# Performance work log

Hardware: AMD Instinct MI355X
Metric: run time of the kernel (lower is better)

## Reference

```python
import jax, jax.numpy as jnp
import numpy as np


def _time_encoding(t, hidden_dim):
    # Sinusoidal continuous-time encoding: t [B,T] -> [B,T,H]
    half = hidden_dim // 2
    freqs = jnp.exp(-jnp.arange(half, dtype=t.dtype) * (np.log(10000.0) / half))
    ang = t[..., None] * freqs  # [B,T,half]
    return jnp.concatenate([jnp.sin(ang), jnp.cos(ang)], axis=-1)


def _gru(x_tbh, w_ih, w_hh, b_ih, b_hh):
    # PyTorch-convention GRU over time-major input [T,B,H]
    B = x_tbh.shape[1]
    H = w_hh.shape[1]
    h0 = jnp.zeros((B, H), x_tbh.dtype)

    def step(h, x):
        gi = x @ w_ih.T + b_ih
        gh = h @ w_hh.T + b_hh
        i_r, i_z, i_n = jnp.split(gi, 3, axis=-1)
        h_r, h_z, h_n = jnp.split(gh, 3, axis=-1)
        r = jax.nn.sigmoid(i_r + h_r)
        z = jax.nn.sigmoid(i_z + h_z)
        n = jnp.tanh(i_n + r * h_n)
        h_new = (1.0 - z) * n + z * h
        return h_new, h_new

    _, ys = jax.lax.scan(step, h0, x_tbh)
    return ys  # [T,B,H]


def setup_inputs():
    key = jax.random.key(0)
    ks = jax.random.split(key, 8)
    B, T, D, H = 32, 256, 64, 128
    x = jax.random.normal(ks[0], (B, T, D), jnp.float32)
    missing_mask = (jax.random.uniform(ks[1], (B, T, D)) < 0.5).astype(jnp.float32)
    visit_time = jnp.cumsum(jax.random.uniform(ks[2], (B, T), jnp.float32) * 2.0, axis=1)
    time_delta = jnp.zeros((B, T), jnp.float32)
    lengths = jax.random.randint(ks[3], (B,), T // 2, T + 1).astype(jnp.int32)
    lengths = lengths.at[0].set(T)  # pad_packed returns max(lengths) steps; pin to T
    sensor_embed = jax.random.normal(ks[4], (D, H), jnp.float32) * 0.02
    k = 1.0 / np.sqrt(H)
    gru_w_ih = jax.random.uniform(ks[5], (3 * H, H), jnp.float32, -k, k)
    gru_w_hh = jax.random.uniform(ks[6], (3 * H, H), jnp.float32, -k, k)
    gru_b_ih = jax.random.uniform(ks[7], (3 * H,), jnp.float32, -k, k)
    gru_b_hh = jnp.zeros((3 * H,), jnp.float32)
    return dict(x=x, missing_mask=missing_mask, visit_time=visit_time,
                time_delta=time_delta, lengths=lengths, sensor_embed=sensor_embed,
                gru_w_ih=gru_w_ih, gru_w_hh=gru_w_hh, gru_b_ih=gru_b_ih, gru_b_hh=gru_b_hh)


def reference(x, missing_mask, visit_time, time_delta, lengths, sensor_embed,
              gru_w_ih, gru_w_hh, gru_b_ih, gru_b_hh):
    B, T, D = x.shape
    H = sensor_embed.shape[1]
    observed = 1.0 - missing_mask                                   # [B,T,D]
    # sensor tokens: per-(t,sensor) embedding scaled by value, zeroed if missing
    sensor_tokens = x[..., None] * sensor_embed[None, None] * observed[..., None]  # [B,T,D,H]
    presence = observed.mean(axis=1)                                # [B,D]
    sim = jax.nn.relu(sensor_embed @ sensor_embed.T)                # [D,D]
    adj = presence[:, :, None] * presence[:, None, :] * sim[None]   # [B,D,D]
    adj = adj + jnp.eye(D, dtype=x.dtype)[None]
    adj = adj / jnp.maximum(adj.sum(axis=-1, keepdims=True), 1e-6)
    graph_tokens = jnp.einsum('bij,btjh->btih', adj, sensor_tokens) # [B,T,D,H]
    visit_repr = graph_tokens.mean(axis=2) + _time_encoding(visit_time, H)  # [B,T,H]
    # dropout is identity in eval mode
    ys = _gru(jnp.swapaxes(visit_repr, 0, 1), gru_w_ih, gru_w_hh, gru_b_ih, gru_b_hh)
    out = jnp.swapaxes(ys, 0, 1)                                    # [B,T,H]
    # pad_packed_sequence semantics: zeros beyond each sequence length
    mask = (jnp.arange(T)[None, :] < lengths[:, None])[..., None]
    return out * mask
```

## Files before the change

kernel.cpp:

```cpp
#include <hip/hip_runtime.h>
#include <hip/hip_bf16.h>

#define B_ 32
#define T_ 256
#define D_ 64
#define H_ 128
#define G_ 384

typedef _Float16 half8 __attribute__((ext_vector_type(8)));
typedef _Float16 half4v __attribute__((ext_vector_type(4)));
typedef float float4v __attribute__((ext_vector_type(4)));

__device__ __forceinline__ float fsigmoid2(float s){
  return __builtin_amdgcn_rcpf(1.0f + __builtin_amdgcn_exp2f(-s));
}
__device__ __forceinline__ float ftanh2(float t){
  return 1.0f - 2.0f*__builtin_amdgcn_rcpf(1.0f + __builtin_amdgcn_exp2f(t));
}
#define LOG2E  1.442695041f
#define LOG2E2 2.885390082f

#define BAR() do{ asm volatile("s_waitcnt lgkmcnt(0)" ::: "memory"); \
                  __builtin_amdgcn_s_barrier(); \
                  asm volatile("" ::: "memory"); } while(0)

__global__ void __launch_bounds__(256) adj_k(const float* mm, const float* E,
                                             float* wcol){
  int b = blockIdx.x;
  int tid = threadIdx.x;
  int d = tid & 63, q = tid >> 6;
  __shared__ float spp[4][64];
  __shared__ float sp[64];
  __shared__ float sE[64*129];
  __shared__ float ssim[64*65];
  __shared__ float srs[64];
  float p = 0.0f;
  for (int t = q*64; t < q*64+64; t++) p += 1.0f - mm[(b*T_ + t)*D_ + d];
  spp[q][d] = p;
  for (int i = tid; i < D_*H_; i += 256){ int r = i >> 7, c = i & 127; sE[r*129+c] = E[i]; }
  __syncthreads();
  if (tid < 64) sp[tid] = (spp[0][tid]+spp[1][tid]+spp[2][tid]+spp[3][tid]) * (1.0f/T_);
  __syncthreads();
  float rowE[128];
  #pragma unroll
  for (int k = 0; k < 128; k++) rowE[k] = sE[d*129+k];
  for (int i = q*16; i < q*16+16; i++){
    float s = 0.0f;
    #pragma unroll
    for (int k = 0; k < 128; k++) s += rowE[k]*sE[i*129+k];
    ssim[d*65+i] = fmaxf(s, 0.0f);
  }
  __syncthreads();
  if (tid < 64){
    float rs = 0.0f;
    for (int j = 0; j < 64; j++) rs += sp[j]*ssim[tid*65+j];
    srs[tid] = fmaxf(sp[tid]*rs + 1.0f, 1e-6f);
  }
  __syncthreads();
  if (tid < 64){
    float s = 0.0f;
    for (int i = 0; i < 64; i++) s += sp[i]*ssim[tid*65+i]/srs[i];
    wcol[b*64 + tid] = sp[tid]*s + 1.0f/srs[tid];
  }
}

#define AVP 72
#define VRP 136
#define SEP 132
__global__ void __launch_bounds__(512,1) gi_k(const float* x, const float* mm,
                                              const float* vt, const float* E,
                                              const float* wih, const float* bih,
                                              const float* bhh, const float* wcol,
                                              _Float16* gi3){
  int bid = blockIdx.x;
  int b = bid >> 3, t0 = (bid & 7)*32;
  int tid = threadIdx.x;
  int w = tid >> 6, l = tid & 63;
  int lq = l >> 4, lm = l & 15;

  __shared__ __align__(16) _Float16 av[32*AVP];
  __shared__ __align__(16) _Float16 vrA[32*VRP];
  __shared__ __align__(16) _Float16 sEl[64*SEP];
  __shared__ float sVt[32];

  {
    int i = tid*4, t = i >> 6, d4 = i & 63;
    long src = (long)(b*T_ + t0 + t)*D_ + d4;
    float4 xv = *(const float4*)&x[src];
    float4 mv = *(const float4*)&mm[src];
    float4 wv = *(const float4*)&wcol[b*D_ + d4];
    half4v h;
    h[0]=(_Float16)(xv.x*(1.0f-mv.x)*wv.x*(1.0f/64));
    h[1]=(_Float16)(xv.y*(1.0f-mv.y)*wv.y*(1.0f/64));
    h[2]=(_Float16)(xv.z*(1.0f-mv.z)*wv.z*(1.0f/64));
    h[3]=(_Float16)(xv.w*(1.0f-mv.w)*wv.w*(1.0f/64));
    *(half4v*)&av[t*AVP + d4] = h;
  }
  {
    int r = tid >> 3, c0 = (tid & 7)*16;
    #pragma unroll
    for (int g = 0; g < 4; g++){
      float4 v = *(const float4*)&E[r*H_ + c0 + g*4];
      half4v h;
      h[0]=(_Float16)v.x; h[1]=(_Float16)v.y; h[2]=(_Float16)v.z; h[3]=(_Float16)v.w;
      *(half4v*)&sEl[r*SEP + c0 + g*4] = h;
    }
  }
  if (tid < 32) sVt[tid] = vt[b*T_ + t0 + tid];
  __syncthreads();

  half8 bE[2];
  #pragma unroll
  for (int kc = 0; kc < 2; kc++){
    half8 f;
    #pragma unroll
    for (int jj = 0; jj < 8; jj++)
      f[jj] = sEl[(kc*32 + lq*8 + jj)*SEP + 16*w + lm];
    bE[kc] = f;
  }

  float4v accA[2] = {{0,0,0,0},{0,0,0,0}};
  #pragma unroll
  for (int kc = 0; kc < 2; kc++){
    #pragma unroll
    for (int mt = 0; mt < 2; mt++){
      half8 a = *(const half8*)&av[(mt*16+lm)*AVP + kc*32 + lq*8];
      accA[mt] = __builtin_amdgcn_mfma_f32_16x16x32_f16(a, bE[kc], accA[mt], 0,0,0);
    }
  }
  {
    int h = 16*w + lm;
    float fr = __expf(-(float)(h & 63) * 0.14391157f);
    #pragma unroll
    for (int mt = 0; mt < 2; mt++){
      #pragma unroll
      for (int r = 0; r < 4; r++){
        int tl = mt*16 + lq*4 + r;
        float ang = sVt[tl] * fr;
        float e = (h < 64) ? __sinf(ang) : __cosf(ang);
        vrA[tl*VRP + h] = (_Float16)(accA[mt][r] + e);
      }
    }
  }
  __syncthreads();

  half8 bW[3][4]; float biW[3];
  #pragma unroll
  for (int q = 0; q < 3; q++){
    int g = 16*(3*w + q) + lm;
    float sc = (g < 2*H_) ? LOG2E : LOG2E2;
    biW[q] = (bih[g] + (g < 2*H_ ? bhh[g] : 0.0f)) * sc;
    #pragma unroll
    for (int kc = 0; kc < 4; kc++){
      const float* src = &wih[(long)g*H_ + kc*32 + lq*8];
      float4 x0 = *(const float4*)src;
      float4 x1 = *(const float4*)(src+4);
      half8 f;
      f[0]=(_Float16)(x0.x*sc); f[1]=(_Float16)(x0.y*sc); f[2]=(_Float16)(x0.z*sc); f[3]=(_Float16)(x0.w*sc);
      f[4]=(_Float16)(x1.x*sc); f[5]=(_Float16)(x1.y*sc); f[6]=(_Float16)(x1.z*sc); f[7]=(_Float16)(x1.w*sc);
      bW[q][kc] = f;
    }
  }
  float4v cB[2][3];
  #pragma unroll
  for (int mt = 0; mt < 2; mt++)
    #pragma unroll
    for (int q = 0; q < 3; q++) cB[mt][q] = (float4v){0,0,0,0};
  #pragma unroll
  for (int kc = 0; kc < 4; kc++){
    #pragma unroll
    for (int mt = 0; mt < 2; mt++){
      half8 a = *(const half8*)&vrA[(mt*16+lm)*VRP + kc*32 + lq*8];
      #pragma unroll
      for (int q = 0; q < 3; q++)
        cB[mt][q] = __builtin_amdgcn_mfma_f32_16x16x32_f16(a, bW[q][kc], cB[mt][q], 0,0,0);
    }
  }
  #pragma unroll
  for (int mt = 0; mt < 2; mt++){
    #pragma unroll
    for (int q = 0; q < 3; q++){
      int g = 16*(3*w + q) + lm;
      int tb = t0 + mt*16 + lq*4;
      half4v hv;
      hv[0]=(_Float16)(cB[mt][q][0] + biW[q]); hv[1]=(_Float16)(cB[mt][q][1] + biW[q]);
      hv[2]=(_Float16)(cB[mt][q][2] + biW[q]); hv[3]=(_Float16)(cB[mt][q][3] + biW[q]);
      *(half4v*)&gi3[((long)(b*G_ + g))*T_ + tb] = hv;
    }
  }
}

__global__ void __launch_bounds__(512,1) gru_k(const _Float16* gi3, const float* whh,
                                               const float* bhh, const int* lengths,
                                               float* out){
  int b = blockIdx.x;
  int tid = threadIdx.x;
  int w = tid >> 6, l = tid & 63;
  int lq = l >> 4;
  int j = 16*w + (l & 15);
  bool gate = (l < 16);
  int len = lengths[b];

  __shared__ __align__(16) _Float16 hb[2][H_];

  half8 bfrag[3][4];
  #pragma unroll
  for (int q = 0; q < 3; q++){
    int row = q*H_ + 16*w + (l & 15);
    float sc = (q == 2) ? LOG2E2 : LOG2E;
    #pragma unroll
    for (int kc = 0; kc < 4; kc++){
      const float* src = &whh[(long)row*H_ + kc*32 + lq*8];
      float4 x0 = *(const float4*)src;
      float4 x1 = *(const float4*)(src+4);
      half8 f;
      f[0]=(_Float16)(x0.x*sc); f[1]=(_Float16)(x0.y*sc); f[2]=(_Float16)(x0.z*sc); f[3]=(_Float16)(x0.w*sc);
      f[4]=(_Float16)(x1.x*sc); f[5]=(_Float16)(x1.y*sc); f[6]=(_Float16)(x1.z*sc); f[7]=(_Float16)(x1.w*sc);
      bfrag[q][kc] = f;
    }
  }
  float bn_ = bhh[2*H_ + j] * LOG2E2;
  const _Float16* pr = gi3 + ((long)b*G_ + j)*T_;
  const _Float16* pz = pr + (long)H_*T_;
  const _Float16* pn = pr + (long)2*H_*T_;

  if (tid < H_){ hb[0][tid] = (_Float16)0.0f; hb[1][tid] = (_Float16)0.0f; }

  half8 prA, pzA, pnA, prB, pzB, pnB;
  prA = *(const half8*)pr; pzA = *(const half8*)pz; pnA = *(const half8*)pn;
  __syncthreads();

  float hval = 0.0f;

  auto substeps = [&](half8 cr, half8 cz, half8 cn, int c){
    float ho[8];
    #pragma unroll
    for (int i = 0; i < 8; i++){
      const int rp = i & 1;
      half8 a0v = *(const half8*)&hb[rp][ 0 + lq*8];
      half8 a1v = *(const half8*)&hb[rp][32 + lq*8];
      half8 a2v = *(const half8*)&hb[rp][64 + lq*8];
      half8 a3v = *(const half8*)&hb[rp][96 + lq*8];
      float4v c0 = {0,0,0,0}, c1 = {0,0,0,0}, c2 = {0,0,0,0};
      c0 = __builtin_amdgcn_mfma_f32_16x16x32_f16(a0v, bfrag[0][0], c0, 0,0,0);
      c1 = __builtin_amdgcn_mfma_f32_16x16x32_f16(a0v, bfrag[1][0], c1, 0,0,0);
      c2 = __builtin_amdgcn_mfma_f32_16x16x32_f16(a0v, bfrag[2][0], c2, 0,0,0);
      c0 = __builtin_amdgcn_mfma_f32_16x16x32_f16(a1v, bfrag[0][1], c0, 0,0,0);
      c1 = __builtin_amdgcn_mfma_f32_16x16x32_f16(a1v, bfrag[1][1], c1, 0,0,0);
      c2 = __builtin_amdgcn_mfma_f32_16x16x32_f16(a1v, bfrag[2][1], c2, 0,0,0);
      c0 = __builtin_amdgcn_mfma_f32_16x16x32_f16(a2v, bfrag[0][2], c0, 0,0,0);
      c1 = __builtin_amdgcn_mfma_f32_16x16x32_f16(a2v, bfrag[1][2], c1, 0,0,0);
      c2 = __builtin_amdgcn_mfma_f32_16x16x32_f16(a2v, bfrag[2][2], c2, 0,0,0);
      c0 = __builtin_amdgcn_mfma_f32_16x16x32_f16(a3v, bfrag[0][3], c0, 0,0,0);
      c1 = __builtin_amdgcn_mfma_f32_16x16x32_f16(a3v, bfrag[1][3], c1, 0,0,0);
      c2 = __builtin_amdgcn_mfma_f32_16x16x32_f16(a3v, bfrag[2][3], c2, 0,0,0);
      float r = fsigmoid2((float)cr[i] + c0[0]);
      float z = fsigmoid2((float)cz[i] + c1[0]);
      float n = ftanh2((float)cn[i] + r*(c2[0] + bn_));
      hval = (1.0f - z)*n + z*hval;
      if (gate){
        hb[rp^1][j] = (_Float16)hval;
        ho[i] = (c*8 + i < len) ? hval : 0.0f;
      }
      BAR();
    }
    if (gate){
      long ob = ((long)b*T_ + c*8)*H_ + j;
      #pragma unroll
      for (int i = 0; i < 8; i++) out[ob + (long)i*H_] = ho[i];
    }
  };

  for (int c = 0; c < 32; c += 2){
    {
      int nb = (c+1)*8;
      prB = *(const half8*)(pr+nb); pzB = *(const half8*)(pz+nb); pnB = *(const half8*)(pn+nb);
    }
    substeps(prA, pzA, pnA, c);
    if (c+2 < 32){
      int nb = (c+2)*8;
      prA = *(const half8*)(pr+nb); pzA = *(const half8*)(pz+nb); pnA = *(const half8*)(pn+nb);
    }
    substeps(prB, pzB, pnB, c+1);
  }
}

extern "C" void kernel_launch(void* const* d_in, const int* in_sizes, int n_in,
                              void* d_out, int out_size, void* d_ws, size_t ws_size,
                              hipStream_t stream) {
  char* base = (char*)d_ws;
  size_t off = 0;
  auto alloc = [&](size_t bytes)->void*{
    void* p = base + off; off = (off + bytes + 255) & ~(size_t)255; return p;
  };
  float*     wcol = (float*)alloc((size_t)B_*D_*4);
  _Float16*  gi3  = (_Float16*)alloc((size_t)B_*G_*T_*2);
  if (off > ws_size) return;

  const float* x   = (const float*)d_in[0];
  const float* mm  = (const float*)d_in[1];
  const float* vt  = (const float*)d_in[2];
  const int*   len = (const int*)d_in[4];
  const float* E   = (const float*)d_in[5];
  const float* wih = (const float*)d_in[6];
  const float* whh = (const float*)d_in[7];
  const float* bih = (const float*)d_in[8];
  const float* bhh = (const float*)d_in[9];

  adj_k<<<dim3(B_),dim3(256),0,stream>>>(mm, E, wcol);
  gi_k<<<dim3(256),dim3(512),0,stream>>>(x, mm, vt, E, wih, bih, bhh, wcol, gi3);
  gru_k<<<dim3(B_),dim3(512),0,stream>>>(gi3, whh, bhh, len, (float*)d_out);
}
```

Measured before the change: 227.7 us.

## Use FP8 scaled MFMA for GRU recurrent matvec to shorten serial step

Quantizes the recurrent weights and hidden state to FP8 with a scale of 16 on each side, undone through the MFMA block scales of 123 (2^-4 each). Each step then issues three 16x16x128 scaled MFMAs in place of twelve f16 16x16x32 MFMAs, and reads the hidden state with one 32-byte LDS load instead of four. It also raises wave priority around the MFMAs and swaps launch_bounds(512,1) for waves_per_eu(2,2). The goal is lower latency per sequential timestep, at the cost of far lower precision in the recurrence, which may break the accuracy tolerance.

Measured after the change: 215.2 us, median of 2. 5.5% less time.

```diff
diff --git a/kernel.cpp b/kernel.cpp
--- a/kernel.cpp
+++ b/kernel.cpp
@@ -10,6 +10,7 @@
 typedef _Float16 half8 __attribute__((ext_vector_type(8)));
 typedef _Float16 half4v __attribute__((ext_vector_type(4)));
 typedef float float4v __attribute__((ext_vector_type(4)));
+typedef int int8v __attribute__((ext_vector_type(8)));
 
 __device__ __forceinline__ float fsigmoid2(float s){
   return __builtin_amdgcn_rcpf(1.0f + __builtin_amdgcn_exp2f(-s));
@@ -190,9 +191,10 @@
   }
 }
 
-__global__ void __launch_bounds__(512,1) gru_k(const _Float16* gi3, const float* whh,
-                                               const float* bhh, const int* lengths,
-                                               float* out){
+__global__ void __attribute__((amdgpu_waves_per_eu(2, 2)))
+__launch_bounds__(512) gru_k(const _Float16* gi3, const float* whh,
+                             const float* bhh, const int* lengths,
+                             float* out){
   int b = blockIdx.x;
   int tid = threadIdx.x;
   int w = tid >> 6, l = tid & 63;
@@ -201,30 +203,30 @@
   bool gate = (l < 16);
   int len = lengths[b];
 
-  __shared__ __align__(16) _Float16 hb[2][H_];
-
-  half8 bfrag[3][4];
+  __shared__ __align__(32) unsigned char hb8[2][H_];
+
+  int8v bf8[3];
   #pragma unroll
   for (int q = 0; q < 3; q++){
     int row = q*H_ + 16*w + (l & 15);
-    float sc = (q == 2) ? LOG2E2 : LOG2E;
-    #pragma unroll
-    for (int kc = 0; kc < 4; kc++){
-      const float* src = &whh[(long)row*H_ + kc*32 + lq*8];
-      float4 x0 = *(const float4*)src;
-      float4 x1 = *(const float4*)(src+4);
-      half8 f;
-      f[0]=(_Float16)(x0.x*sc); f[1]=(_Float16)(x0.y*sc); f[2]=(_Float16)(x0.z*sc); f[3]=(_Float16)(x0.w*sc);
-      f[4]=(_Float16)(x1.x*sc); f[5]=(_Float16)(x1.y*sc); f[6]=(_Float16)(x1.z*sc); f[7]=(_Float16)(x1.w*sc);
-      bfrag[q][kc] = f;
-    }
+    float sc16 = ((q == 2) ? LOG2E2 : LOG2E) * 16.0f;
+    const float* src = &whh[(long)row*H_ + lq*32];
+    int8v f;
+    #pragma unroll
+    for (int d = 0; d < 8; d++){
+      float4 v = *(const float4*)(src + d*4);
+      int pk = __builtin_amdgcn_cvt_pk_fp8_f32(v.x*sc16, v.y*sc16, 0, false);
+      pk = __builtin_amdgcn_cvt_pk_fp8_f32(v.z*sc16, v.w*sc16, pk, true);
+      f[d] = pk;
+    }
+    bf8[q] = f;
   }
   float bn_ = bhh[2*H_ + j] * LOG2E2;
   const _Float16* pr = gi3 + ((long)b*G_ + j)*T_;
   const _Float16* pz = pr + (long)H_*T_;
   const _Float16* pn = pr + (long)2*H_*T_;
 
-  if (tid < H_){ hb[0][tid] = (_Float16)0.0f; hb[1][tid] = (_Float16)0.0f; }
+  if (tid < H_){ hb8[0][tid] = 0; hb8[1][tid] = 0; }
 
   half8 prA, pzA, pnA, prB, pzB, pnB;
   prA = *(const half8*)pr; pzA = *(const half8*)pz; pnA = *(const half8*)pn;
@@ -237,29 +239,20 @@
     #pragma unroll
     for (int i = 0; i < 8; i++){
       const int rp = i & 1;
-      half8 a0v = *(const half8*)&hb[rp][ 0 + lq*8];
-      half8 a1v = *(const half8*)&hb[rp][32 + lq*8];
-      half8 a2v = *(const half8*)&hb[rp][64 + lq*8];
-      half8 a3v = *(const half8*)&hb[rp][96 + lq*8];
+      int8v av = *(const int8v*)&hb8[rp][lq*32];
       float4v c0 = {0,0,0,0}, c1 = {0,0,0,0}, c2 = {0,0,0,0};
-      c0 = __builtin_amdgcn_mfma_f32_16x16x32_f16(a0v, bfrag[0][0], c0, 0,0,0);
-      c1 = __builtin_amdgcn_mfma_f32_16x16x32_f16(a0v, bfrag[1][0], c1, 0,0,0);
-      c2 = __builtin_amdgcn_mfma_f32_16x16x32_f16(a0v, bfrag[2][0], c2, 0,0,0);
-      c0 = __builtin_amdgcn_mfma_f32_16x16x32_f16(a1v, bfrag[0][1], c0, 0,0,0);
-      c1 = __builtin_amdgcn_mfma_f32_16x16x32_f16(a1v, bfrag[1][1], c1, 0,0,0);
-      c2 = __builtin_amdgcn_mfma_f32_16x16x32_f16(a1v, bfrag[2][1], c2, 0,0,0);
-      c0 = __builtin_amdgcn_mfma_f32_16x16x32_f16(a2v, bfrag[0][2], c0, 0,0,0);
-      c1 = __builtin_amdgcn_mfma_f32_16x16x32_f16(a2v, bfrag[1][2], c1, 0,0,0);
-      c2 = __builtin_amdgcn_mfma_f32_16x16x32_f16(a2v, bfrag[2][2], c2, 0,0,0);
-      c0 = __builtin_amdgcn_mfma_f32_16x16x32_f16(a3v, bfrag[0][3], c0, 0,0,0);
-      c1 = __builtin_amdgcn_mfma_f32_16x16x32_f16(a3v, bfrag[1][3], c1, 0,0,0);
-      c2 = __builtin_amdgcn_mfma_f32_16x16x32_f16(a3v, bfrag[2][3], c2, 0,0,0);
+      __builtin_amdgcn_s_setprio(1);
+      c0 = __builtin_amdgcn_mfma_scale_f32_16x16x128_f8f6f4(av, bf8[0], c0, 0, 0, 0, 123, 0, 123);
+      c1 = __builtin_amdgcn_mfma_scale_f32_16x16x128_f8f6f4(av, bf8[1], c1, 0, 0, 0, 123, 0, 123);
+      c2 = __builtin_amdgcn_mfma_scale_f32_16x16x128_f8f6f4(av, bf8[2], c2, 0, 0, 0, 123, 0, 123);
+      __builtin_amdgcn_s_setprio(0);
       float r = fsigmoid2((float)cr[i] + c0[0]);
       float z = fsigmoid2((float)cz[i] + c1[0]);
       float n = ftanh2((float)cn[i] + r*(c2[0] + bn_));
       hval = (1.0f - z)*n + z*hval;
       if (gate){
-        hb[rp^1][j] = (_Float16)hval;
+        int hq = __builtin_amdgcn_cvt_pk_fp8_f32(hval*16.0f, hval*16.0f, 0, false);
+        hb8[rp^1][j] = (unsigned char)(hq & 0xff);
         ho[i] = (c*8 + i < len) ? hval : 0.0f;
       }
       BAR();
```
